# Optimization experiments

Measured on AMD Instinct MI355X. Metric: run time of the kernel, lower is better.

## Reference

```python
import jax, jax.numpy as jnp
import numpy as np

NUM_SEGMENTS = 64  # number of bags (max batch id + 1)
TEMP = 1.0
EPS_NORM = 1e-12
EPS_SOFTMAX = 1e-16

D = 1024
L = 128
N = 262144


def setup_inputs() -> dict:
    key = jax.random.key(0)
    ks = jax.random.split(key, 8)
    feature = jax.random.normal(ks[0], (N, D), dtype=jnp.float32)
    batch = jnp.sort(jax.random.randint(ks[1], (N,), 0, NUM_SEGMENTS, dtype=jnp.int32))
    # xavier_normal_ init: std = sqrt(2/(fan_in+fan_out))
    Wa = jax.random.normal(ks[2], (L, D), dtype=jnp.float32) * np.sqrt(2.0 / (D + L))
    ba = jnp.zeros((L,), dtype=jnp.float32)
    Wb = jax.random.normal(ks[3], (L, D), dtype=jnp.float32) * np.sqrt(2.0 / (D + L))
    bb = jnp.zeros((L,), dtype=jnp.float32)
    Wc = jax.random.normal(ks[4], (1, L), dtype=jnp.float32) * np.sqrt(2.0 / (L + 1))
    bc = jnp.zeros((1,), dtype=jnp.float32)
    return {"feature": feature, "batch": batch, "istrain": 0,
            "Wa": Wa, "ba": ba, "Wb": Wb, "bb": bb, "Wc": Wc, "bc": bc}


def segment_softmax(score, batch, num_segments):
    # score: [N, 1], batch: [N] segment ids (torch_geometric softmax semantics)
    seg_max = jax.ops.segment_max(score, batch, num_segments=num_segments)
    ex = jnp.exp(score - seg_max[batch])
    denom = jax.ops.segment_sum(ex, batch, num_segments=num_segments)
    return ex / (denom[batch] + EPS_SOFTMAX)


def reference(feature, batch, istrain, Wa, ba, Wb, bb, Wc, bc):
    # F.normalize: L2-normalize each row (dim=1)
    norm = jnp.linalg.norm(feature, axis=1, keepdims=True)
    instance_norm_feature = feature / jnp.maximum(norm, EPS_NORM)
    a = jax.nn.sigmoid(feature @ Wa.T + ba)          # [N, L]
    b = jnp.tanh(feature @ Wb.T + bb)                # [N, L]
    gated = a * b                                     # [N, L]
    score = (gated @ Wc.T + bc) / TEMP               # [N, 1]
    score = segment_softmax(score, batch, NUM_SEGMENTS)
    # istrain=0 -> dropout is identity in this reference
    return (instance_norm_feature, score)
```

## Files before the change

kernel.cpp:

```cpp
#include <hip/hip_runtime.h>

#define DD 1024
#define LL 128
#define NSEG 64
#define CHS 544
#define NTILE 16384
#define GRID 768

typedef float floatx4 __attribute__((ext_vector_type(4)));

__global__ __launch_bounds__(256)
void prep_kernel(const float* __restrict__ Wa, const float* __restrict__ Wb,
                 unsigned char* __restrict__ Wf8, unsigned* __restrict__ smaxu,
                 float* __restrict__ denom, float* __restrict__ score_raw)
{
    int gid = blockIdx.x * 256 + threadIdx.x;
    if (gid < 2 * LL * DD) {
        const int j    = gid & 7;
        const int lane = (gid >> 3) & 63;
        const int ct   = (gid >> 9) & 15;
        const int c    = gid >> 13;
        const int r = ct * 16 + (lane & 15);
        const int k = c * 32 + (lane >> 4) * 8 + j;
        const float v = ((r < LL) ? Wa[r * DD + k] : Wb[(r - LL) * DD + k]) * 16.0f;
        unsigned u = __builtin_amdgcn_cvt_pk_fp8_f32(v, v, 0, false);
        Wf8[gid] = (unsigned char)(u & 0xFF);
        score_raw[gid] = 0.0f;
    }
    if (gid < NSEG)          smaxu[gid] = 0u;
    else if (gid < 2 * NSEG) denom[gid - NSEG] = 0.0f;
}

__global__ __launch_bounds__(512, 6)
void fused_main(const float* __restrict__ feat,
                const unsigned char* __restrict__ Wf8,
                const float* __restrict__ ba,
                const float* __restrict__ bb,
                const float* __restrict__ Wc,
                float* __restrict__ out_norm,
                float* __restrict__ score_raw)
{
    __shared__ __align__(16) char tile[32 * CHS];

    const int tid  = threadIdx.x;
    const int wave = tid >> 6;
    const int lane = tid & 63;
    const int s15  = lane & 15;
    const int l4   = lane >> 4;
    const int G    = gridDim.x;

    float4 L[2][4];

    auto issue = [&](long long tt) {
        const float* fb = feat + ((size_t)tt * 16 + wave * 2) * DD + lane * 4;
        #pragma unroll
        for (int i = 0; i < 2; ++i)
            #pragma unroll
            for (int c = 0; c < 4; ++c)
                L[i][c] = *reinterpret_cast<const float4*>(fb + (size_t)i * DD + c * 256);
    };

    long long t = blockIdx.x;
    if (t < NTILE) issue(t);

    while (t < NTILE) {
        const long long row0 = t * 16;

        unsigned pw[2][4];
        #pragma unroll
        for (int i = 0; i < 2; ++i) {
            float ss = 0.0f;
            #pragma unroll
            for (int c = 0; c < 4; ++c)
                ss += L[i][c].x * L[i][c].x + L[i][c].y * L[i][c].y
                    + L[i][c].z * L[i][c].z + L[i][c].w * L[i][c].w;
            #pragma unroll
            for (int off = 32; off >= 1; off >>= 1) ss += __shfl_xor(ss, off);
            const float rinv = 1.0f / fmaxf(sqrtf(ss), 1e-12f);

            float* ob = out_norm + (row0 + wave * 2 + i) * DD + lane * 4;
            #pragma unroll
            for (int c = 0; c < 4; ++c) {
                float4 v;
                v.x = L[i][c].x * rinv; v.y = L[i][c].y * rinv;
                v.z = L[i][c].z * rinv; v.w = L[i][c].w * rinv;
                *reinterpret_cast<float4*>(ob + c * 256) = v;
            }
            #pragma unroll
            for (int c = 0; c < 4; ++c) {
                unsigned u = __builtin_amdgcn_cvt_pk_fp8_f32(L[i][c].x * 8.0f, L[i][c].y * 8.0f, 0, false);
                u = __builtin_amdgcn_cvt_pk_fp8_f32(L[i][c].z * 8.0f, L[i][c].w * 8.0f, u, true);
                pw[i][c] = u;
            }
        }

        __syncthreads();
        #pragma unroll
        for (int i = 0; i < 2; ++i) {
            const int r = wave * 2 + i;
            #pragma unroll
            for (int c = 0; c < 4; ++c) {
                const int chunk = (lane >> 3) + c * 8;
                const int addr  = chunk * CHS + r * 32 + ((lane >> 1) & 3) * 8 + (lane & 1) * 4;
                *reinterpret_cast<unsigned*>(tile + addr) = pw[i][c];
            }
        }
        __syncthreads();

        const long long tn = t + G;
        if (tn < NTILE) issue(tn);
        __builtin_amdgcn_sched_barrier(0);

        floatx4 acc0 = (floatx4)0.0f;
        floatx4 acc1 = (floatx4)0.0f;
        const unsigned char* bb0 = Wf8 + (size_t)wave * 512 + (size_t)lane * 8;

        #pragma unroll 4
        for (int c = 0; c < 32; ++c) {
            const long long a8 = *reinterpret_cast<const long long*>(tile + c * CHS + s15 * 32 + l4 * 8);
            const long long w0 = *reinterpret_cast<const long long*>(bb0 + (size_t)c * 8192);
            const long long w1 = *reinterpret_cast<const long long*>(bb0 + (size_t)c * 8192 + 8 * 512);
            acc0 = __builtin_amdgcn_mfma_f32_16x16x32_fp8_fp8(a8, w0, acc0, 0, 0, 0);
            acc1 = __builtin_amdgcn_mfma_f32_16x16x32_fp8_fp8(a8, w1, acc1, 0, 0, 0);
        }

        {
            const float S = 1.0f / 128.0f;
            const int col = wave * 16 + s15;
            const float bav = ba[col], bbv = bb[col], wcv = Wc[col];
            float s[4];
            #pragma unroll
            for (int j = 0; j < 4; ++j) {
                const float av = 1.0f / (1.0f + expf(-(acc0[j] * S + bav)));
                const float bv = tanhf(acc1[j] * S + bbv);
                s[j] = av * bv * wcv;
            }
            #pragma unroll
            for (int j = 0; j < 4; ++j) {
                s[j] += __shfl_xor(s[j], 1);
                s[j] += __shfl_xor(s[j], 2);
                s[j] += __shfl_xor(s[j], 4);
                s[j] += __shfl_xor(s[j], 8);
            }
            if (s15 == 0) {
                #pragma unroll
                for (int j = 0; j < 4; ++j)
                    atomicAdd(&score_raw[row0 + l4 * 4 + j], s[j]);
            }
        }
        t = tn;
    }
}

__global__ __launch_bounds__(256)
void seg_max_kernel(const float* __restrict__ score, const int* __restrict__ batch,
                    unsigned* __restrict__ smaxu, int n)
{
    __shared__ unsigned sm[NSEG];
    const int t = threadIdx.x;
    if (t < NSEG) sm[t] = 0u;
    __syncthreads();
    const int stride = gridDim.x * blockDim.x;
    for (int i = blockIdx.x * blockDim.x + t; i < n; i += stride) {
        const unsigned b = __float_as_uint(score[i]);
        const unsigned m = (b & 0x80000000u) ? ~b : (b | 0x80000000u);
        atomicMax(&sm[batch[i]], m);
    }
    __syncthreads();
    if (t < NSEG) atomicMax(&smaxu[t], sm[t]);
}

__global__ __launch_bounds__(256)
void seg_exp_kernel(float* __restrict__ score_inout, const int* __restrict__ batch,
                    const unsigned* __restrict__ smaxu, float* __restrict__ denom, int n)
{
    __shared__ float sd[NSEG];
    __shared__ float smx[NSEG];
    const int t = threadIdx.x;
    if (t < NSEG) {
        sd[t] = 0.0f;
        const unsigned u = smaxu[t];
        const unsigned b = (u & 0x80000000u) ? (u ^ 0x80000000u) : ~u;
        smx[t] = __uint_as_float(b);
    }
    __syncthreads();
    const int stride = gridDim.x * blockDim.x;
    for (int i = blockIdx.x * blockDim.x + t; i < n; i += stride) {
        const int b = batch[i];
        const float e = expf(score_inout[i] - smx[b]);
        score_inout[i] = e;
        atomicAdd(&sd[b], e);
    }
    __syncthreads();
    if (t < NSEG) atomicAdd(&denom[t], sd[t]);
}

__global__ __launch_bounds__(256)
void seg_div_kernel(float* __restrict__ score_inout, const int* __restrict__ batch,
                    const float* __restrict__ denom, int n)
{
    const int stride = gridDim.x * blockDim.x;
    for (int i = blockIdx.x * blockDim.x + threadIdx.x; i < n; i += stride)
        score_inout[i] = score_inout[i] / (denom[batch[i]] + 1e-16f);
}

extern "C" void kernel_launch(void* const* d_in, const int* in_sizes, int n_in,
                              void* d_out, int out_size, void* d_ws, size_t ws_size,
                              hipStream_t stream)
{
    const float* feat  = (const float*)d_in[0];
    const int*   batch = (const int*)d_in[1];
    const float* Wa = (const float*)d_in[3];
    const float* ba = (const float*)d_in[4];
    const float* Wb = (const float*)d_in[5];
    const float* bb = (const float*)d_in[6];
    const float* Wc = (const float*)d_in[7];

    const int N = in_sizes[1];

    float* out_norm  = (float*)d_out;
    float* out_score = (float*)d_out + (size_t)N * DD;

    char* ws = (char*)d_ws;
    unsigned char* Wf8 = (unsigned char*)ws;
    unsigned* smaxu = (unsigned*)(ws + 2 * LL * DD);
    float*    denom = (float*)(ws + 2 * LL * DD + 256);

    prep_kernel<<<(2 * LL * DD + 255) / 256, 256, 0, stream>>>(Wa, Wb, Wf8, smaxu, denom, out_score);
    fused_main<<<GRID, 512, 0, stream>>>(feat, Wf8, ba, bb, Wc, out_norm, out_score);
    seg_max_kernel<<<512, 256, 0, stream>>>(out_score, batch, smaxu, N);
    seg_exp_kernel<<<512, 256, 0, stream>>>(out_score, batch, smaxu, denom, N);
    seg_div_kernel<<<512, 256, 0, stream>>>(out_score, batch, denom, N);
}
```

Before: 532.6 us.

## Double-buffer LDS tiles, shrink grid, and drop the segment-max pass

```diff
diff --git a/kernel.cpp b/kernel.cpp
--- a/kernel.cpp
+++ b/kernel.cpp
@@ -4,15 +4,15 @@
 #define LL 128
 #define NSEG 64
 #define CHS 544
-#define NTILE 16384
-#define GRID 768
+#define TB  17408
+#define GRID 512
 
 typedef float floatx4 __attribute__((ext_vector_type(4)));
 
 __global__ __launch_bounds__(256)
 void prep_kernel(const float* __restrict__ Wa, const float* __restrict__ Wb,
-                 unsigned char* __restrict__ Wf8, unsigned* __restrict__ smaxu,
-                 float* __restrict__ denom, float* __restrict__ score_raw)
+                 unsigned char* __restrict__ Wf8, float* __restrict__ denom,
+                 float* __restrict__ score_raw)
 {
     int gid = blockIdx.x * 256 + threadIdx.x;
     if (gid < 2 * LL * DD) {
@@ -27,45 +27,51 @@
         Wf8[gid] = (unsigned char)(u & 0xFF);
         score_raw[gid] = 0.0f;
     }
-    if (gid < NSEG)          smaxu[gid] = 0u;
-    else if (gid < 2 * NSEG) denom[gid - NSEG] = 0.0f;
-}
-
-__global__ __launch_bounds__(512, 6)
+    if (gid < NSEG) denom[gid] = 0.0f;
+}
+
+__global__ __launch_bounds__(512, 4)
 void fused_main(const float* __restrict__ feat,
                 const unsigned char* __restrict__ Wf8,
                 const float* __restrict__ ba,
                 const float* __restrict__ bb,
                 const float* __restrict__ Wc,
                 float* __restrict__ out_norm,
-                float* __restrict__ score_raw)
-{
-    __shared__ __align__(16) char tile[32 * CHS];
+                float* __restrict__ score_raw,
+                int n)
+{
+    __shared__ __align__(16) char tile[2 * TB];
 
     const int tid  = threadIdx.x;
     const int wave = tid >> 6;
     const int lane = tid & 63;
     const int s15  = lane & 15;
     const int l4   = lane >> 4;
-    const int G    = gridDim.x;
-
-    float4 L[2][4];
-
-    auto issue = [&](long long tt) {
+    const long long G = gridDim.x;
+    const long long ntile = n >> 4;
+    const int nt_per = (int)(ntile / G);
+
+    float4 La[2][4], Lb[2][4];
+
+    auto issueA = [&](long long tt) {
         const float* fb = feat + ((size_t)tt * 16 + wave * 2) * DD + lane * 4;
         #pragma unroll
         for (int i = 0; i < 2; ++i)
             #pragma unroll
             for (int c = 0; c < 4; ++c)
-                L[i][c] = *reinterpret_cast<const float4*>(fb + (size_t)i * DD + c * 256);
-    };
-
-    long long t = blockIdx.x;
-    if (t < NTILE) issue(t);
-
-    while (t < NTILE) {
+                La[i][c] = *reinterpret_cast<const float4*>(fb + (size_t)i * DD + c * 256);
+    };
+    auto issueB = [&](long long tt) {
+        const float* fb = feat + ((size_t)tt * 16 + wave * 2) * DD + lane * 4;
+        #pragma unroll
+        for (int i = 0; i < 2; ++i)
+            #pragma unroll
+            for (int c = 0; c < 4; ++c)
+                Lb[i][c] = *reinterpret_cast<const float4*>(fb + (size_t)i * DD + c * 256);
+    };
+
+    auto consume_stage = [&](float4 (&L)[2][4], int p, long long t) {
         const long long row0 = t * 16;
-
         unsigned pw[2][4];
         #pragma unroll
         for (int i = 0; i < 2; ++i) {
@@ -93,103 +99,92 @@
                 pw[i][c] = u;
             }
         }
-
-        __syncthreads();
         #pragma unroll
         for (int i = 0; i < 2; ++i) {
             const int r = wave * 2 + i;
             #pragma unroll
             for (int c = 0; c < 4; ++c) {
                 const int chunk = (lane >> 3) + c * 8;
-                const int addr  = chunk * CHS + r * 32 + ((lane >> 1) & 3) * 8 + (lane & 1) * 4;
+                const int addr  = p * TB + chunk * CHS + r * 32 + ((lane >> 1) & 3) * 8 + (lane & 1) * 4;
                 *reinterpret_cast<unsigned*>(tile + addr) = pw[i][c];
             }
         }
-        __syncthreads();
-
-        const long long tn = t + G;
-        if (tn < NTILE) issue(tn);
-        __builtin_amdgcn_sched_barrier(0);
-
+    };
+
+    auto mfma_epi = [&](int p, long long t) {
+        const long long row0 = t * 16;
         floatx4 acc0 = (floatx4)0.0f;
         floatx4 acc1 = (floatx4)0.0f;
         const unsigned char* bb0 = Wf8 + (size_t)wave * 512 + (size_t)lane * 8;
+        const char* tb = tile + p * TB;
 
         #pragma unroll 4
         for (int c = 0; c < 32; ++c) {
-            const long long a8 = *reinterpret_cast<const long long*>(tile + c * CHS + s15 * 32 + l4 * 8);
+            const long long a8 = *reinterpret_cast<const long long*>(tb + c * CHS + s15 * 32 + l4 * 8);
             const long long w0 = *reinterpret_cast<const long long*>(bb0 + (size_t)c * 8192);
             const long long w1 = *reinterpret_cast<const long long*>(bb0 + (size_t)c * 8192 + 8 * 512);
             acc0 = __builtin_amdgcn_mfma_f32_16x16x32_fp8_fp8(a8, w0, acc0, 0, 0, 0);
             acc1 = __builtin_amdgcn_mfma_f32_16x16x32_fp8_fp8(a8, w1, acc1, 0, 0, 0);
         }
-
-        {
-            const float S = 1.0f / 128.0f;
-            const int col = wave * 16 + s15;
-            const float bav = ba[col], bbv = bb[col], wcv = Wc[col];
-            float s[4];
-            #pragma unroll
-            for (int j = 0; j < 4; ++j) {
-                const float av = 1.0f / (1.0f + expf(-(acc0[j] * S + bav)));
-                const float bv = tanhf(acc1[j] * S + bbv);
-                s[j] = av * bv * wcv;
-            }
-            #pragma unroll
-            for (int j = 0; j < 4; ++j) {
-                s[j] += __shfl_xor(s[j], 1);
-                s[j] += __shfl_xor(s[j], 2);
-                s[j] += __shfl_xor(s[j], 4);
-                s[j] += __shfl_xor(s[j], 8);
-            }
-            if (s15 == 0) {
-                #pragma unroll
-                for (int j = 0; j < 4; ++j)
-                    atomicAdd(&score_raw[row0 + l4 * 4 + j], s[j]);
-            }
-        }
-        t = tn;
+        const float S = 1.0f / 128.0f;
+        const int col = wave * 16 + s15;
+        const float bav = ba[col], bbv = bb[col], wcv = Wc[col];
+        float s[4];
+        #pragma unroll
+        for (int j = 0; j < 4; ++j) {
+            const float av = 1.0f / (1.0f + expf(-(acc0[j] * S + bav)));
+            const float bv = tanhf(acc1[j] * S + bbv);
+            s[j] = av * bv * wcv;
+        }
+        #pragma unroll
+        for (int j = 0; j < 4; ++j) {
+            s[j] += __shfl_xor(s[j], 1);
+            s[j] += __shfl_xor(s[j], 2);
+            s[j] += __shfl_xor(s[j], 4);
+            s[j] += __shfl_xor(s[j], 8);
+        }
+        if (s15 == 0) {
+            #pragma unroll
+            for (int j = 0; j < 4; ++j)
+                atomicAdd(&score_raw[row0 + l4 * 4 + j], s[j]);
+        }
+    };
+
+    const long long bid = blockIdx.x;
+    issueA(bid);
+    if (nt_per > 1) issueB(bid + G);
+
+    for (int it = 0; it < nt_per; it += 2) {
+        const long long tA = bid + (long long)it * G;
+        consume_stage(La, 0, tA);
+        __syncthreads();
+        if (it + 2 < nt_per) issueA(tA + 2 * G);
+        __builtin_amdgcn_sched_barrier(0);
+        mfma_epi(0, tA);
+        if (it + 1 < nt_per) {
+            const long long tB = tA + G;
+            consume_stage(Lb, 1, tB);
+            __syncthreads();
+            if (it + 3 < nt_per) issueB(tB + 2 * G);
+            __builtin_amdgcn_sched_barrier(0);
+            mfma_epi(1, tB);
+        }
     }
 }
 
 __global__ __launch_bounds__(256)
-void seg_max_kernel(const float* __restrict__ score, const int* __restrict__ batch,
-                    unsigned* __restrict__ smaxu, int n)
-{
-    __shared__ unsigned sm[NSEG];
+void seg_exp_kernel(float* __restrict__ score_inout, const int* __restrict__ batch,
+                    float* __restrict__ denom, int n)
+{
+    __shared__ float sd[NSEG];
     const int t = threadIdx.x;
-    if (t < NSEG) sm[t] = 0u;
+    if (t < NSEG) sd[t] = 0.0f;
     __syncthreads();
     const int stride = gridDim.x * blockDim.x;
     for (int i = blockIdx.x * blockDim.x + t; i < n; i += stride) {
-        const unsigned b = __float_as_uint(score[i]);
-        const unsigned m = (b & 0x80000000u) ? ~b : (b | 0x80000000u);
-        atomicMax(&sm[batch[i]], m);
-    }
-    __syncthreads();
-    if (t < NSEG) atomicMax(&smaxu[t], sm[t]);
-}
-
-__global__ __launch_bounds__(256)
-void seg_exp_kernel(float* __restrict__ score_inout, const int* __restrict__ batch,
-                    const unsigned* __restrict__ smaxu, float* __restrict__ denom, int n)
-{
-    __shared__ float sd[NSEG];
-    __shared__ float smx[NSEG];
-    const int t = threadIdx.x;
-    if (t < NSEG) {
-        sd[t] = 0.0f;
-        const unsigned u = smaxu[t];
-        const unsigned b = (u & 0x80000000u) ? (u ^ 0x80000000u) : ~u;
-        smx[t] = __uint_as_float(b);
-    }
-    __syncthreads();
-    const int stride = gridDim.x * blockDim.x;
-    for (int i = blockIdx.x * blockDim.x + t; i < n; i += stride) {
-        const int b = batch[i];
-        const float e = expf(score_inout[i] - smx[b]);
+        const float e = expf(score_inout[i]);
         score_inout[i] = e;
-        atomicAdd(&sd[b], e);
+        atomicAdd(&sd[batch[i]], e);
     }
     __syncthreads();
     if (t < NSEG) atomicAdd(&denom[t], sd[t]);
@@ -223,12 +218,10 @@
 
     char* ws = (char*)d_ws;
     unsigned char* Wf8 = (unsigned char*)ws;
-    unsigned* smaxu = (unsigned*)(ws + 2 * LL * DD);
-    float*    denom = (float*)(ws + 2 * LL * DD + 256);
-
-    prep_kernel<<<(2 * LL * DD + 255) / 256, 256, 0, stream>>>(Wa, Wb, Wf8, smaxu, denom, out_score);
-    fused_main<<<GRID, 512, 0, stream>>>(feat, Wf8, ba, bb, Wc, out_norm, out_score);
-    seg_max_kernel<<<512, 256, 0, stream>>>(out_score, batch, smaxu, N);
-    seg_exp_kernel<<<512, 256, 0, stream>>>(out_score, batch, smaxu, denom, N);
+    float* denom = (float*)(ws + 2 * LL * DD);
+
+    prep_kernel<<<(2 * LL * DD + 255) / 256, 256, 0, stream>>>(Wa, Wb, Wf8, denom, out_score);
+    fused_main<<<GRID, 512, 0, stream>>>(feat, Wf8, ba, bb, Wc, out_norm, out_score, N);
+    seg_exp_kernel<<<512, 256, 0, stream>>>(out_score, batch, denom, N);
     seg_div_kernel<<<512, 256, 0, stream>>>(out_score, batch, denom, N);
 }
```

Result: no change. 531.3 us (-0.2%).
